# Optimization experiments

Hardware: AMD Instinct MI355X
Metric: run time of the kernel (lower is better)

The kernel has to match this reference:

```python
import jax, jax.numpy as jnp
import numpy as np

PC_RANGE = np.array([-51.2, -51.2, -5.0, 51.2, 51.2, 3.0], dtype=np.float32)
IMG_H, IMG_W = 256.0, 704.0
EPS = 1e-5


def bilinear_sample(feat, grid):
    """torch.grid_sample(bilinear, padding_mode='zeros', align_corners=False).
    feat: [C, H, W]; grid: [M, 2] with (x, y) in [-1, 1]. Returns [C, M]."""
    C, H, W = feat.shape
    x = ((grid[:, 0] + 1.0) * W - 1.0) * 0.5
    y = ((grid[:, 1] + 1.0) * H - 1.0) * 0.5
    x0 = jnp.floor(x); y0 = jnp.floor(y)
    x1 = x0 + 1.0;     y1 = y0 + 1.0
    wx1 = x - x0; wx0 = 1.0 - wx1
    wy1 = y - y0; wy0 = 1.0 - wy1

    def gather(xi, yi, w):
        valid = (xi >= 0) & (xi <= W - 1) & (yi >= 0) & (yi <= H - 1)
        xc = jnp.clip(xi, 0, W - 1).astype(jnp.int32)
        yc = jnp.clip(yi, 0, H - 1).astype(jnp.int32)
        v = feat[:, yc, xc]                      # [C, M]
        return v * (w * valid.astype(w.dtype))[None, :]

    return (gather(x0, y0, wx0 * wy0) + gather(x1, y0, wx1 * wy0)
            + gather(x0, y1, wx0 * wy1) + gather(x1, y1, wx1 * wy1))


def setup_inputs() -> dict:
    key = jax.random.key(0)
    k1, k2, k3, k4 = jax.random.split(key, 4)
    reference_points = jax.random.uniform(k1, (1, 4, 128, 128, 3), dtype=jnp.float32)
    feats0 = jax.random.normal(k2, (1, 6, 128, 32, 88), dtype=jnp.float32)
    feats1 = jax.random.normal(k3, (1, 6, 128, 16, 44), dtype=jnp.float32)
    lidar2img = jax.random.normal(k4, (1, 6, 4, 4), dtype=jnp.float32)
    return {"reference_points": reference_points, "feats0": feats0,
            "feats1": feats1, "lidar2img": lidar2img}


def reference(reference_points, feats0, feats1, lidar2img):
    pc = jnp.asarray(PC_RANGE)
    B, P, Hb, Wb, _ = reference_points.shape
    Q = Hb * Wb
    N = lidar2img.shape[1]
    # 'b p h w d' -> 'b (h w) p d' (T=1 squeezed)
    rp = reference_points.transpose(0, 2, 3, 1, 4).reshape(B, Q, P, 3)
    rp = rp * (pc[3:] - pc[:3]) + pc[:3]                     # denormalize
    pts = jnp.concatenate([rp, jnp.ones_like(rp[..., :1])], axis=-1)  # [B,Q,P,4]
    cam = jnp.einsum('bnij,bqpj->bnqpi', lidar2img, pts)     # [B,N,Q,P,4]
    z = cam[..., 2]
    u = cam[..., 0] / (jnp.maximum(z, EPS) * IMG_W)
    v = cam[..., 1] / (jnp.maximum(z, EPS) * IMG_H)
    mask = (z > EPS) & (u > 0.0) & (u < 1.0) & (v > 0.0) & (v < 1.0)  # [B,N,Q,P]
    grid = jnp.stack([u * 2.0 - 1.0, v * 2.0 - 1.0], axis=-1)  # [B,N,Q,P,2]
    grid_flat = grid.reshape(B * N, Q * P, 2)

    sample = jax.vmap(bilinear_sample)   # over B*N
    acc = None
    for feat in (feats0, feats1):
        C, Hl, Wl = feat.shape[2], feat.shape[3], feat.shape[4]
        s = sample(feat.reshape(B * N, C, Hl, Wl), grid_flat)  # [B*N, C, Q*P]
        acc = s if acc is None else acc + s
    sampled = acc / 2.0                                       # mean over 2 levels
    C = feats0.shape[2]
    sampled = sampled.reshape(B, N, C, Q, P)
    m = mask.astype(sampled.dtype)[:, :, None, :, :]          # [B,N,1,Q,P]
    num = jnp.sum(sampled * m, axis=1)                        # [B,C,Q,P]
    den = jnp.maximum(jnp.sum(m, axis=1), 1.0)
    out = (num / den).transpose(0, 2, 3, 1)                   # [B,Q,P,C]
    return out
```

## Files before the change

### kernel.cpp

```cpp
#include <hip/hip_runtime.h>

#define C_CH 128

__global__ __launch_bounds__(256) void transpose_both(
    const float* __restrict__ f0, const float* __restrict__ f1,
    float* __restrict__ o0, float* __restrict__ o1) {
  __shared__ float tile[32][33];
  int n = blockIdx.z;
  int lev = (blockIdx.x >= 88) ? 1 : 0;
  int xt = lev ? (blockIdx.x - 88) : blockIdx.x;
  int HW = lev ? 704 : 2816;
  const float* src = (lev ? f1 : f0) + (size_t)n * C_CH * HW;
  float* dst = (lev ? o1 : o0) + (size_t)n * C_CH * HW;
  int hw0 = xt * 32;
  int c0  = blockIdx.y * 32;
  #pragma unroll
  for (int i = threadIdx.y; i < 32; i += 8) {
    int c  = c0 + i;
    int hw = hw0 + threadIdx.x;
    if (hw < HW) tile[i][threadIdx.x] = src[(size_t)c * HW + hw];
  }
  __syncthreads();
  #pragma unroll
  for (int i = threadIdx.y; i < 32; i += 8) {
    int hw = hw0 + i;
    int c  = c0 + threadIdx.x;
    if (hw < HW) dst[(size_t)hw * C_CH + c] = tile[threadIdx.x][i];
  }
}

__global__ __launch_bounds__(256) void bev_main(
    const float* __restrict__ rp,
    const float* __restrict__ f0t,
    const float* __restrict__ f1t,
    const float* __restrict__ l2i,
    float* __restrict__ out)
{
  __shared__ int   s_off[8][6][2][4];
  __shared__ float s_wt [8][6][2][4];
  __shared__ float s_flag[8][6];

  int tid = threadIdx.x;
  int pt0 = blockIdx.x * 8;

  if (tid < 48) {
    int lp = tid / 6;
    int n  = tid - lp * 6;
    int pt = pt0 + lp;
    int p = pt & 3, q = pt >> 2, h = q >> 7, w = q & 127;
    const float* rpp = rp + ((size_t)((p * 128 + h) * 128 + w)) * 3;
    float X = rpp[0] * 102.4f - 51.2f;
    float Y = rpp[1] * 102.4f - 51.2f;
    float Z = rpp[2] * 8.0f - 5.0f;
    const float* M = l2i + n * 16;
    float cx = fmaf(M[0], X, fmaf(M[1], Y, fmaf(M[2],  Z, M[3])));
    float cy = fmaf(M[4], X, fmaf(M[5], Y, fmaf(M[6],  Z, M[7])));
    float cz = fmaf(M[8], X, fmaf(M[9], Y, fmaf(M[10], Z, M[11])));
    float dz = fmaxf(cz, 1e-5f);
    float u = cx / (dz * 704.0f);
    float v = cy / (dz * 256.0f);
    bool m = (cz > 1e-5f) && (u > 0.0f) && (u < 1.0f) && (v > 0.0f) && (v < 1.0f);
    s_flag[lp][n] = m ? 1.0f : 0.0f;
    if (m) {
      float gx = u * 2.0f - 1.0f;
      float gy = v * 2.0f - 1.0f;
      #pragma unroll
      for (int lev = 0; lev < 2; ++lev) {
        const int H = lev ? 16 : 32, W = lev ? 44 : 88;
        const int base = (lev ? n * 16 * 44 : n * 32 * 88) * C_CH;
        float x = ((gx + 1.0f) * (float)W - 1.0f) * 0.5f;
        float y = ((gy + 1.0f) * (float)H - 1.0f) * 0.5f;
        float x0f = floorf(x), y0f = floorf(y);
        int x0 = (int)x0f, y0 = (int)y0f;
        int x1 = x0 + 1, y1 = y0 + 1;
        float wx1 = x - x0f, wx0 = 1.0f - wx1;
        float wy1 = y - y0f, wy0 = 1.0f - wy1;
        float vx0 = (x0 >= 0 && x0 < W) ? 1.f : 0.f;
        float vx1 = (x1 >= 0 && x1 < W) ? 1.f : 0.f;
        float vy0 = (y0 >= 0 && y0 < H) ? 1.f : 0.f;
        float vy1 = (y1 >= 0 && y1 < H) ? 1.f : 0.f;
        int cx0 = min(max(x0, 0), W - 1), cx1 = min(max(x1, 0), W - 1);
        int cy0 = min(max(y0, 0), H - 1), cy1 = min(max(y1, 0), H - 1);
        s_off[lp][n][lev][0] = base + (cy0 * W + cx0) * C_CH;
        s_off[lp][n][lev][1] = base + (cy0 * W + cx1) * C_CH;
        s_off[lp][n][lev][2] = base + (cy1 * W + cx0) * C_CH;
        s_off[lp][n][lev][3] = base + (cy1 * W + cx1) * C_CH;
        s_wt[lp][n][lev][0] = wx0 * wy0 * vx0 * vy0;
        s_wt[lp][n][lev][1] = wx1 * wy0 * vx1 * vy0;
        s_wt[lp][n][lev][2] = wx0 * wy1 * vx0 * vy1;
        s_wt[lp][n][lev][3] = wx1 * wy1 * vx1 * vy1;
      }
    }
  }
  __syncthreads();

  int lane = tid & 31;
  int grp  = tid >> 5;
  int c = lane << 2;
  float4 acc = make_float4(0.f, 0.f, 0.f, 0.f);
  float cnt = 0.f;
  #pragma unroll
  for (int n = 0; n < 6; ++n) {
    float flag = s_flag[grp][n];
    cnt += flag;
    if (flag != 0.0f) {
      #pragma unroll
      for (int t = 0; t < 4; ++t) {
        float4 val = *reinterpret_cast<const float4*>(f0t + s_off[grp][n][0][t] + c);
        float wgt = s_wt[grp][n][0][t];
        acc.x = fmaf(val.x, wgt, acc.x);
        acc.y = fmaf(val.y, wgt, acc.y);
        acc.z = fmaf(val.z, wgt, acc.z);
        acc.w = fmaf(val.w, wgt, acc.w);
      }
      #pragma unroll
      for (int t = 0; t < 4; ++t) {
        float4 val = *reinterpret_cast<const float4*>(f1t + s_off[grp][n][1][t] + c);
        float wgt = s_wt[grp][n][1][t];
        acc.x = fmaf(val.x, wgt, acc.x);
        acc.y = fmaf(val.y, wgt, acc.y);
        acc.z = fmaf(val.z, wgt, acc.z);
        acc.w = fmaf(val.w, wgt, acc.w);
      }
    }
  }
  float s = 0.5f / fmaxf(cnt, 1.0f);
  int pt = pt0 + grp;
  *reinterpret_cast<float4*>(out + (size_t)pt * C_CH + c) =
      make_float4(acc.x * s, acc.y * s, acc.z * s, acc.w * s);
}

__global__ __launch_bounds__(256) void bev_fallback(
    const float* __restrict__ rp, const float* __restrict__ f0,
    const float* __restrict__ f1, const float* __restrict__ l2i,
    float* __restrict__ out) {
  int lane = threadIdx.x & 31;
  int grp  = threadIdx.x >> 5;
  int pt   = blockIdx.x * 8 + grp;
  int p = pt & 3, q = pt >> 2, h = q >> 7, w = q & 127;
  int c = lane << 2;
  const float* rpp = rp + ((size_t)((p * 128 + h) * 128 + w)) * 3;
  float X = rpp[0] * 102.4f - 51.2f;
  float Y = rpp[1] * 102.4f - 51.2f;
  float Z = rpp[2] * 8.0f - 5.0f;
  float4 acc = make_float4(0.f, 0.f, 0.f, 0.f);
  float cnt = 0.0f;
  for (int n = 0; n < 6; ++n) {
    const float* M = l2i + n * 16;
    float cx = M[0] * X + M[1] * Y + M[2]  * Z + M[3];
    float cy = M[4] * X + M[5] * Y + M[6]  * Z + M[7];
    float cz = M[8] * X + M[9] * Y + M[10] * Z + M[11];
    float dz = fmaxf(cz, 1e-5f);
    float u = cx / (dz * 704.0f);
    float v = cy / (dz * 256.0f);
    if (!((cz > 1e-5f) && (u > 0.f) && (u < 1.f) && (v > 0.f) && (v < 1.f))) continue;
    cnt += 1.0f;
    float gx = u * 2.0f - 1.0f, gy = v * 2.0f - 1.0f;
    for (int lev = 0; lev < 2; ++lev) {
      const int H = lev ? 16 : 32, W = lev ? 44 : 88;
      const float* f = lev ? f1 : f0;
      size_t HW = (size_t)H * W;
      const float* b0 = f + (size_t)n * C_CH * HW + (size_t)c * HW;
      float x = ((gx + 1.0f) * (float)W - 1.0f) * 0.5f;
      float y = ((gy + 1.0f) * (float)H - 1.0f) * 0.5f;
      float x0f = floorf(x), y0f = floorf(y);
      int x0 = (int)x0f, y0 = (int)y0f, x1 = x0 + 1, y1 = y0 + 1;
      float wx1 = x - x0f, wx0 = 1.0f - wx1;
      float wy1 = y - y0f, wy0 = 1.0f - wy1;
      int xs[4] = {x0, x1, x0, x1}, ys[4] = {y0, y0, y1, y1};
      float ws4[4] = {wx0 * wy0, wx1 * wy0, wx0 * wy1, wx1 * wy1};
      for (int t = 0; t < 4; ++t) {
        if (xs[t] < 0 || xs[t] >= W || ys[t] < 0 || ys[t] >= H) continue;
        size_t off = (size_t)ys[t] * W + xs[t];
        float wgt = ws4[t];
        acc.x = fmaf(b0[off], wgt, acc.x);
        acc.y = fmaf(b0[HW + off], wgt, acc.y);
        acc.z = fmaf(b0[2 * HW + off], wgt, acc.z);
        acc.w = fmaf(b0[3 * HW + off], wgt, acc.w);
      }
    }
  }
  float s = 0.5f / fmaxf(cnt, 1.0f);
  *reinterpret_cast<float4*>(out + (size_t)pt * C_CH + c) =
      make_float4(acc.x * s, acc.y * s, acc.z * s, acc.w * s);
}

extern "C" void kernel_launch(void* const* d_in, const int* in_sizes, int n_in,
                              void* d_out, int out_size, void* d_ws, size_t ws_size,
                              hipStream_t stream) {
  const float* rp  = (const float*)d_in[0];
  const float* f0  = (const float*)d_in[1];
  const float* f1  = (const float*)d_in[2];
  const float* l2i = (const float*)d_in[3];
  float* out = (float*)d_out;

  const size_t n0 = (size_t)6 * 128 * 32 * 88;
  const size_t n1 = (size_t)6 * 128 * 16 * 44;
  const size_t need = (n0 + n1) * sizeof(float);

  if (ws_size >= need) {
    float* f0t = (float*)d_ws;
    float* f1t = f0t + n0;
    transpose_both<<<dim3(110, 4, 6), dim3(32, 8, 1), 0, stream>>>(f0, f1, f0t, f1t);
    bev_main<<<dim3(8192), dim3(256), 0, stream>>>(rp, f0t, f1t, l2i, out);
  } else {
    bev_fallback<<<dim3(8192), dim3(256), 0, stream>>>(rp, f0, f1, l2i, out);
  }
}
```

Baseline: 89.92 us.

## Store transposed features as fp16 and gather eight channels per lane

The transpose kernel now writes both feature levels into a single fp16 channel-last buffer. The main kernel gathers 8 half values (16 bytes) per lane, so 16 lanes cover 128 channels, and each block handles 16 points instead of 8, which halves the grid. This halves the gather and workspace traffic and unifies the level loop into 8 taps. It introduces fp16 rounding error in the sampled features, which may affect tolerance.

```diff
diff --git a/kernel.cpp b/kernel.cpp
--- a/kernel.cpp
+++ b/kernel.cpp
@@ -1,49 +1,49 @@
 #include <hip/hip_runtime.h>
 
 #define C_CH 128
-
-__global__ __launch_bounds__(256) void transpose_both(
+typedef __attribute__((ext_vector_type(8))) _Float16 half8;
+
+__global__ __launch_bounds__(256) void transpose_both_f16(
     const float* __restrict__ f0, const float* __restrict__ f1,
-    float* __restrict__ o0, float* __restrict__ o1) {
+    _Float16* __restrict__ o) {
   __shared__ float tile[32][33];
   int n = blockIdx.z;
   int lev = (blockIdx.x >= 88) ? 1 : 0;
   int xt = lev ? (blockIdx.x - 88) : blockIdx.x;
   int HW = lev ? 704 : 2816;
   const float* src = (lev ? f1 : f0) + (size_t)n * C_CH * HW;
-  float* dst = (lev ? o1 : o0) + (size_t)n * C_CH * HW;
+  _Float16* dst = o + (lev ? (size_t)6 * C_CH * 2816 + (size_t)n * C_CH * 704
+                           : (size_t)n * C_CH * 2816);
   int hw0 = xt * 32;
   int c0  = blockIdx.y * 32;
   #pragma unroll
   for (int i = threadIdx.y; i < 32; i += 8) {
-    int c  = c0 + i;
     int hw = hw0 + threadIdx.x;
-    if (hw < HW) tile[i][threadIdx.x] = src[(size_t)c * HW + hw];
+    if (hw < HW) tile[i][threadIdx.x] = src[(size_t)(c0 + i) * HW + hw];
   }
   __syncthreads();
   #pragma unroll
   for (int i = threadIdx.y; i < 32; i += 8) {
     int hw = hw0 + i;
-    int c  = c0 + threadIdx.x;
-    if (hw < HW) dst[(size_t)hw * C_CH + c] = tile[threadIdx.x][i];
-  }
-}
-
-__global__ __launch_bounds__(256) void bev_main(
+    if (hw < HW)
+      dst[(size_t)hw * C_CH + c0 + threadIdx.x] = (_Float16)tile[threadIdx.x][i];
+  }
+}
+
+__global__ __launch_bounds__(256) void bev_main_f16(
     const float* __restrict__ rp,
-    const float* __restrict__ f0t,
-    const float* __restrict__ f1t,
+    const _Float16* __restrict__ ft,
     const float* __restrict__ l2i,
     float* __restrict__ out)
 {
-  __shared__ int   s_off[8][6][2][4];
-  __shared__ float s_wt [8][6][2][4];
-  __shared__ float s_flag[8][6];
+  __shared__ int   s_off[16][6][8];
+  __shared__ float s_wt [16][6][8];
+  __shared__ float s_flag[16][6];
 
   int tid = threadIdx.x;
-  int pt0 = blockIdx.x * 8;
-
-  if (tid < 48) {
+  int pt0 = blockIdx.x * 16;
+
+  if (tid < 96) {
     int lp = tid / 6;
     int n  = tid - lp * 6;
     int pt = pt0 + lp;
@@ -67,7 +67,8 @@
       #pragma unroll
       for (int lev = 0; lev < 2; ++lev) {
         const int H = lev ? 16 : 32, W = lev ? 44 : 88;
-        const int base = (lev ? n * 16 * 44 : n * 32 * 88) * C_CH;
+        const int base = lev ? (6 * 2816 * C_CH + n * 704 * C_CH)
+                             : (n * 2816 * C_CH);
         float x = ((gx + 1.0f) * (float)W - 1.0f) * 0.5f;
         float y = ((gy + 1.0f) * (float)H - 1.0f) * 0.5f;
         float x0f = floorf(x), y0f = floorf(y);
@@ -81,23 +82,23 @@
         float vy1 = (y1 >= 0 && y1 < H) ? 1.f : 0.f;
         int cx0 = min(max(x0, 0), W - 1), cx1 = min(max(x1, 0), W - 1);
         int cy0 = min(max(y0, 0), H - 1), cy1 = min(max(y1, 0), H - 1);
-        s_off[lp][n][lev][0] = base + (cy0 * W + cx0) * C_CH;
-        s_off[lp][n][lev][1] = base + (cy0 * W + cx1) * C_CH;
-        s_off[lp][n][lev][2] = base + (cy1 * W + cx0) * C_CH;
-        s_off[lp][n][lev][3] = base + (cy1 * W + cx1) * C_CH;
-        s_wt[lp][n][lev][0] = wx0 * wy0 * vx0 * vy0;
-        s_wt[lp][n][lev][1] = wx1 * wy0 * vx1 * vy0;
-        s_wt[lp][n][lev][2] = wx0 * wy1 * vx0 * vy1;
-        s_wt[lp][n][lev][3] = wx1 * wy1 * vx1 * vy1;
+        s_off[lp][n][lev * 4 + 0] = base + (cy0 * W + cx0) * C_CH;
+        s_off[lp][n][lev * 4 + 1] = base + (cy0 * W + cx1) * C_CH;
+        s_off[lp][n][lev * 4 + 2] = base + (cy1 * W + cx0) * C_CH;
+        s_off[lp][n][lev * 4 + 3] = base + (cy1 * W + cx1) * C_CH;
+        s_wt[lp][n][lev * 4 + 0] = wx0 * wy0 * vx0 * vy0;
+        s_wt[lp][n][lev * 4 + 1] = wx1 * wy0 * vx1 * vy0;
+        s_wt[lp][n][lev * 4 + 2] = wx0 * wy1 * vx0 * vy1;
+        s_wt[lp][n][lev * 4 + 3] = wx1 * wy1 * vx1 * vy1;
       }
     }
   }
   __syncthreads();
 
-  int lane = tid & 31;
-  int grp  = tid >> 5;
-  int c = lane << 2;
-  float4 acc = make_float4(0.f, 0.f, 0.f, 0.f);
+  int lane = tid & 15;
+  int grp  = tid >> 4;
+  const _Float16* ftc = ft + (lane << 3);
+  float acc[8] = {0.f, 0.f, 0.f, 0.f, 0.f, 0.f, 0.f, 0.f};
   float cnt = 0.f;
   #pragma unroll
   for (int n = 0; n < 6; ++n) {
@@ -105,29 +106,23 @@
     cnt += flag;
     if (flag != 0.0f) {
       #pragma unroll
-      for (int t = 0; t < 4; ++t) {
-        float4 val = *reinterpret_cast<const float4*>(f0t + s_off[grp][n][0][t] + c);
-        float wgt = s_wt[grp][n][0][t];
-        acc.x = fmaf(val.x, wgt, acc.x);
-        acc.y = fmaf(val.y, wgt, acc.y);
-        acc.z = fmaf(val.z, wgt, acc.z);
-        acc.w = fmaf(val.w, wgt, acc.w);
-      }
-      #pragma unroll
-      for (int t = 0; t < 4; ++t) {
-        float4 val = *reinterpret_cast<const float4*>(f1t + s_off[grp][n][1][t] + c);
-        float wgt = s_wt[grp][n][1][t];
-        acc.x = fmaf(val.x, wgt, acc.x);
-        acc.y = fmaf(val.y, wgt, acc.y);
-        acc.z = fmaf(val.z, wgt, acc.z);
-        acc.w = fmaf(val.w, wgt, acc.w);
+      for (int t = 0; t < 8; ++t) {
+        int off = s_off[grp][n][t];
+        float wgt = s_wt[grp][n][t];
+        half8 val = *reinterpret_cast<const half8*>(ftc + off);
+        #pragma unroll
+        for (int j = 0; j < 8; ++j)
+          acc[j] = fmaf((float)val[j], wgt, acc[j]);
       }
     }
   }
   float s = 0.5f / fmaxf(cnt, 1.0f);
   int pt = pt0 + grp;
-  *reinterpret_cast<float4*>(out + (size_t)pt * C_CH + c) =
-      make_float4(acc.x * s, acc.y * s, acc.z * s, acc.w * s);
+  float* op = out + (size_t)pt * C_CH + (lane << 3);
+  *reinterpret_cast<float4*>(op) =
+      make_float4(acc[0] * s, acc[1] * s, acc[2] * s, acc[3] * s);
+  *reinterpret_cast<float4*>(op + 4) =
+      make_float4(acc[4] * s, acc[5] * s, acc[6] * s, acc[7] * s);
 }
 
 __global__ __launch_bounds__(256) void bev_fallback(
@@ -194,15 +189,13 @@
   const float* l2i = (const float*)d_in[3];
   float* out = (float*)d_out;
 
-  const size_t n0 = (size_t)6 * 128 * 32 * 88;
-  const size_t n1 = (size_t)6 * 128 * 16 * 44;
-  const size_t need = (n0 + n1) * sizeof(float);
+  const size_t n_elems = (size_t)6 * C_CH * 2816 + (size_t)6 * C_CH * 704;
+  const size_t need = n_elems * sizeof(_Float16);
 
   if (ws_size >= need) {
-    float* f0t = (float*)d_ws;
-    float* f1t = f0t + n0;
-    transpose_both<<<dim3(110, 4, 6), dim3(32, 8, 1), 0, stream>>>(f0, f1, f0t, f1t);
-    bev_main<<<dim3(8192), dim3(256), 0, stream>>>(rp, f0t, f1t, l2i, out);
+    _Float16* ftp = (_Float16*)d_ws;
+    transpose_both_f16<<<dim3(110, 4, 6), dim3(32, 8, 1), 0, stream>>>(f0, f1, ftp);
+    bev_main_f16<<<dim3(4096), dim3(256), 0, stream>>>(rp, ftp, l2i, out);
   } else {
     bev_fallback<<<dim3(8192), dim3(256), 0, stream>>>(rp, f0, f1, l2i, out);
   }
```

After: 90.77 us. About the same (+0.9%).
